# Kernel optimization log

Hardware: AMD Instinct MI355X
Metric: run time of the kernel (lower is better)

## Reference

```python
import jax, jax.numpy as jnp
import numpy as np

BN_EPS = 1e-5

def bn(x, gamma, beta):
    # x: [N, C]; BatchNorm2d over (batch, spatial) == node axis here (training-mode batch stats)
    mu = x.mean(axis=0, keepdims=True)
    var = x.var(axis=0, keepdims=True)
    return (x - mu) * jax.lax.rsqrt(var + BN_EPS) * gamma + beta

def octree_conv(x, neigh, W):
    # x: [N, Cin]; neigh: [N, K] with values in [0, N], N == empty neighbor
    # W: [K, Cin, Cout]. Sparse octree conv = neighbor gather + contraction.
    xp = jnp.concatenate([x, jnp.zeros((1, x.shape[1]), x.dtype)], axis=0)  # zero row for empties
    g = xp[neigh]                                  # [N, K, Cin]
    return jnp.einsum('nkc,kcd->nd', g, W)         # [N, Cout]

def setup_inputs() -> dict:
    key = jax.random.key(0)
    ks = jax.random.split(key, 8)
    N, Cin, Cout, Cb, K = 60000, 256, 512, 128, 27
    s = 0.05
    return {
        'x': jax.random.normal(ks[0], (1, Cin, N, 1), jnp.float32),
        'neigh': jax.random.randint(ks[1], (N, K), 0, N + 1),
        'W1a': jax.random.normal(ks[2], (Cb, Cin), jnp.float32) * s,
        'g1a': jnp.ones((Cb,), jnp.float32), 'b1a': jnp.zeros((Cb,), jnp.float32),
        'W3': jax.random.normal(ks[3], (K, Cb, Cb), jnp.float32) * s,
        'g3': jnp.ones((Cb,), jnp.float32), 'b3': jnp.zeros((Cb,), jnp.float32),
        'W1b': jax.random.normal(ks[4], (Cout, Cb), jnp.float32) * s,
        'g1b': jnp.ones((Cout,), jnp.float32), 'b1b': jnp.zeros((Cout,), jnp.float32),
        'Wc': jax.random.normal(ks[5], (Cout, Cin), jnp.float32) * s,
        'gc': jnp.ones((Cout,), jnp.float32), 'bc': jnp.zeros((Cout,), jnp.float32),
    }

def reference(x, neigh, W1a, g1a, b1a, W3, g3, b3, W1b, g1b, b1b, Wc, gc, bc):
    h = jnp.squeeze(x, axis=(0, 3)).T                         # [N, Cin]
    c1 = jax.nn.relu(bn(h @ W1a.T, g1a, b1a))                 # 1x1 conv + BN + ReLU -> [N, Cb]
    c2 = jax.nn.relu(bn(octree_conv(c1, neigh, W3), g3, b3))  # sparse 3x3 octree conv + BN + ReLU
    c3 = bn(c2 @ W1b.T, g1b, b1b)                             # 1x1 conv + BN -> [N, Cout]
    sc = bn(h @ Wc.T, gc, bc)                                 # shortcut 1x1 conv + BN (Cin != Cout)
    out = jax.nn.relu(c3 + sc)
    return out.T[None, :, :, None]                            # [1, Cout, N, 1]
```

## Files before the change

kernel.cpp:

```cpp
#include <hip/hip_runtime.h>


typedef __bf16 bf16x8 __attribute__((ext_vector_type(8)));
typedef float f32x4 __attribute__((ext_vector_type(4)));
typedef unsigned short u16x8 __attribute__((ext_vector_type(8)));
typedef unsigned short u16x4 __attribute__((ext_vector_type(4)));

__device__ __forceinline__ unsigned short f2bfu(float f) {
  union { float f; unsigned u; } v; v.f = f;
  unsigned r = v.u + 0x7fffu + ((v.u >> 16) & 1u);
  return (unsigned short)(r >> 16);
}
__device__ __forceinline__ float bfu2f(unsigned short s) {
  union { unsigned u; float f; } v; v.u = ((unsigned)s) << 16;
  return v.f;
}

__device__ __forceinline__ void gload_lds16(const unsigned short* g, unsigned short* l) {
  __builtin_amdgcn_global_load_lds(
      (const __attribute__((address_space(1))) unsigned int*)(unsigned long long)g,
      (__attribute__((address_space(3))) unsigned int*)(unsigned int)(unsigned long long)l,
      16, 0, 0);
}

__global__ __launch_bounds__(256) void prep_weights(
    const float* __restrict__ W1a, const float* __restrict__ W3,
    const float* __restrict__ W1b, const float* __restrict__ Wc,
    unsigned short* __restrict__ w1a, unsigned short* __restrict__ w3t,
    unsigned short* __restrict__ w1b, unsigned short* __restrict__ wc) {
  int i = blockIdx.x * 256 + threadIdx.x;
  int stride = gridDim.x * 256;
  for (; i < 442368; i += stride) {
    if (i < 32768)  w1a[i] = f2bfu(W1a[i]);
    if (i < 65536)  w1b[i] = f2bfu(W1b[i]);
    if (i < 131072) wc[i]  = f2bfu(Wc[i]);
    int k = i >> 14, rr = i & 16383;
    int d = rr >> 7, c = rr & 127;
    w3t[i] = f2bfu(W3[(k << 14) + (c << 7) + d]);
  }
}

__global__ __launch_bounds__(256) void transpose_x(
    const float* __restrict__ x, unsigned short* __restrict__ h, int M) {
  __shared__ float tile[64][65];
  int n0 = blockIdx.x * 64, c0 = blockIdx.y * 64;
  int t = threadIdx.x;
  int nl = t & 63;
#pragma unroll
  for (int i = 0; i < 16; ++i) {
    int cl = i * 4 + (t >> 6);
    int n = n0 + nl;
    tile[cl][nl] = (n < M) ? x[(size_t)(c0 + cl) * M + n] : 0.f;
  }
  __syncthreads();
  int cl = t & 63;
#pragma unroll
  for (int i = 0; i < 16; ++i) {
    int nl2 = i * 4 + (t >> 6);
    int n = n0 + nl2;
    h[(size_t)n * 256 + c0 + cl] = f2bfu(tile[cl][nl2]);
  }
}

__global__ __launch_bounds__(256) void gemm128(
    const unsigned short* __restrict__ A, const unsigned short* __restrict__ W,
    unsigned short* __restrict__ C, float* __restrict__ partials,
    int M, int Kd, int Nc) {
  __shared__ unsigned short sA[2][128 * 64];
  __shared__ unsigned short sB[2][128 * 64];
  __shared__ float sStat[4][2][128];
  int t = threadIdx.x, wave = t >> 6, lane = t & 63;
  int n0 = blockIdx.x * 128, m0 = blockIdx.y * 128;
  int wr = wave >> 1, wcc = wave & 1;
  int l4 = lane >> 4, lc = lane & 15, lc7 = lc & 7;
  int lrow = lane >> 3, lch = lane & 7;
  f32x4 acc[4][4] = {};
  const int np = Kd >> 6;

  auto STAGE = [&](int p, int buf) {
    int k0 = p << 6;
#pragma unroll
    for (int i = 0; i < 4; ++i) {
      int row = wave * 32 + i * 8 + lrow;
      int sc = lch ^ (row & 7);
      gload_lds16(A + (size_t)(m0 + row) * Kd + k0 + sc * 8, &sA[buf][(wave * 32 + i * 8) * 64]);
    }
#pragma unroll
    for (int i = 0; i < 4; ++i) {
      int row = wave * 32 + i * 8 + lrow;
      int sc = lch ^ (row & 7);
      gload_lds16(W + (size_t)(n0 + row) * Kd + k0 + sc * 8, &sB[buf][(wave * 32 + i * 8) * 64]);
    }
  };
  auto COMPUTE = [&](int buf) {
#pragma unroll
    for (int kk = 0; kk < 2; ++kk) {
      bf16x8 af[4], bfr[4];
#pragma unroll
      for (int mi = 0; mi < 4; ++mi) {
        int row = wr * 64 + mi * 16 + lc;
        int chunk = (kk * 4 + l4) ^ lc7;
        af[mi] = __builtin_bit_cast(bf16x8, *(const u16x8*)(&sA[buf][row * 64 + chunk * 8]));
      }
#pragma unroll
      for (int ni = 0; ni < 4; ++ni) {
        int row = wcc * 64 + ni * 16 + lc;
        int chunk = (kk * 4 + l4) ^ lc7;
        bfr[ni] = __builtin_bit_cast(bf16x8, *(const u16x8*)(&sB[buf][row * 64 + chunk * 8]));
      }
      __builtin_amdgcn_s_setprio(1);
#pragma unroll
      for (int mi = 0; mi < 4; ++mi)
#pragma unroll
        for (int ni = 0; ni < 4; ++ni)
          acc[mi][ni] = __builtin_amdgcn_mfma_f32_16x16x32_bf16(af[mi], bfr[ni], acc[mi][ni], 0, 0, 0);
      __builtin_amdgcn_s_setprio(0);
    }
  };

  STAGE(0, 0);
  for (int p = 0; p < np; ++p) {
    int cur = p & 1;
    if (p < np - 1) {
      STAGE(p + 1, cur ^ 1);
      asm volatile("s_waitcnt vmcnt(8)" ::: "memory");
    } else {
      asm volatile("s_waitcnt vmcnt(0)" ::: "memory");
    }
    __builtin_amdgcn_sched_barrier(0);
    __builtin_amdgcn_s_barrier();
    __builtin_amdgcn_sched_barrier(0);
    COMPUTE(cur);
    __builtin_amdgcn_sched_barrier(0);
    __builtin_amdgcn_s_barrier();
  }

#pragma unroll
  for (int ni = 0; ni < 4; ++ni) {
    float s = 0.f, q = 0.f;
    int col = wcc * 64 + ni * 16 + lc;
#pragma unroll
    for (int mi = 0; mi < 4; ++mi)
#pragma unroll
      for (int j = 0; j < 4; ++j) {
        int n = m0 + wr * 64 + mi * 16 + l4 * 4 + j;
        unsigned short u = f2bfu(acc[mi][ni][j]);
        if (n < M) C[(size_t)n * Nc + n0 + col] = u;
        float v = bfu2f(u);
        s += v; q += v * v;
      }
    s += __shfl_xor(s, 16); s += __shfl_xor(s, 32);
    q += __shfl_xor(q, 16); q += __shfl_xor(q, 32);
    if (lane < 16) {
      sStat[wave][0][col] = s;
      sStat[wave][1][col] = q;
    }
  }
  __syncthreads();
  if (t < 128) {
    int wcs = t >> 6;
    float s = sStat[wcs][0][t] + sStat[wcs + 2][0][t];
    float q = sStat[wcs][1][t] + sStat[wcs + 2][1][t];
    partials[(size_t)blockIdx.y * (2 * Nc) + n0 + t] = s;
    partials[(size_t)blockIdx.y * (2 * Nc) + Nc + n0 + t] = q;
  }
}

__global__ __launch_bounds__(512, 4) void octree_gemm(
    const unsigned short* __restrict__ c1, const int* __restrict__ neigh,
    const unsigned short* __restrict__ w3t, unsigned short* __restrict__ c2p,
    float* __restrict__ partials, int M) {
  __shared__ unsigned short sA[2][128 * 64];
  __shared__ unsigned short sB[2][128 * 64];
  __shared__ union {
    unsigned short nidx[128 * 27];
    float stat[8][2][128];
  } u;
  int t = threadIdx.x, wave = t >> 6, lane = t & 63;
  int m0 = blockIdx.x * 128;
  for (int i = t; i < 128 * 27; i += 512) {
    int row = i / 27;
    u.nidx[i] = (unsigned short)((m0 + row < M) ? neigh[(size_t)m0 * 27 + i] : M);
  }
  __syncthreads();

  int wr = wave >> 1, wcc = wave & 1;
  int l4 = lane >> 4, lc = lane & 15, lc7 = lc & 7;
  int lrow = lane >> 3, lch = lane & 7;
  f32x4 acc[2][4] = {};

  auto STAGE = [&](int p, int buf) {
    int k = p >> 1, c0 = (p & 1) << 6;
#pragma unroll
    for (int i = 0; i < 2; ++i) {
      int row = wave * 16 + i * 8 + lrow;
      int nr = u.nidx[row * 27 + k];
      int sc = lch ^ (row & 7);
      gload_lds16(c1 + ((size_t)nr << 7) + c0 + sc * 8, &sA[buf][(wave * 16 + i * 8) * 64]);
    }
    const unsigned short* wk = w3t + ((size_t)k << 14);
#pragma unroll
    for (int i = 0; i < 2; ++i) {
      int row = wave * 16 + i * 8 + lrow;
      int sc = lch ^ (row & 7);
      gload_lds16(wk + ((size_t)row << 7) + c0 + sc * 8, &sB[buf][(wave * 16 + i * 8) * 64]);
    }
  };
  auto COMPUTE = [&](int buf) {
#pragma unroll
    for (int kk = 0; kk < 2; ++kk) {
      bf16x8 af[2], bfr[4];
#pragma unroll
      for (int mi = 0; mi < 2; ++mi) {
        int row = wr * 32 + mi * 16 + lc;
        int chunk = (kk * 4 + l4) ^ lc7;
        af[mi] = __builtin_bit_cast(bf16x8, *(const u16x8*)(&sA[buf][row * 64 + chunk * 8]));
      }
#pragma unroll
      for (int ni = 0; ni < 4; ++ni) {
        int row = wcc * 64 + ni * 16 + lc;
        int chunk = (kk * 4 + l4) ^ lc7;
        bfr[ni] = __builtin_bit_cast(bf16x8, *(const u16x8*)(&sB[buf][row * 64 + chunk * 8]));
      }
      __builtin_amdgcn_s_setprio(1);
#pragma unroll
      for (int mi = 0; mi < 2; ++mi)
#pragma unroll
        for (int ni = 0; ni < 4; ++ni)
          acc[mi][ni] = __builtin_amdgcn_mfma_f32_16x16x32_bf16(af[mi], bfr[ni], acc[mi][ni], 0, 0, 0);
      __builtin_amdgcn_s_setprio(0);
    }
  };

  STAGE(0, 0);
  for (int p = 0; p < 54; ++p) {
    int cur = p & 1;
    if (p < 53) {
      STAGE(p + 1, cur ^ 1);
      asm volatile("s_waitcnt vmcnt(4)" ::: "memory");
    } else {
      asm volatile("s_waitcnt vmcnt(0)" ::: "memory");
    }
    __builtin_amdgcn_sched_barrier(0);
    __builtin_amdgcn_s_barrier();
    __builtin_amdgcn_sched_barrier(0);
    COMPUTE(cur);
    __builtin_amdgcn_sched_barrier(0);
    __builtin_amdgcn_s_barrier();
  }

#pragma unroll
  for (int ni = 0; ni < 4; ++ni) {
    float s = 0.f, q = 0.f;
    int col = wcc * 64 + ni * 16 + lc;
#pragma unroll
    for (int mi = 0; mi < 2; ++mi)
#pragma unroll
      for (int j = 0; j < 4; ++j) {
        int n = m0 + wr * 32 + mi * 16 + l4 * 4 + j;
        unsigned short uo = f2bfu(acc[mi][ni][j]);
        if (n < M) c2p[(size_t)n * 128 + col] = uo;
        float v = bfu2f(uo);
        s += v; q += v * v;
      }
    s += __shfl_xor(s, 16); s += __shfl_xor(s, 32);
    q += __shfl_xor(q, 16); q += __shfl_xor(q, 32);
    if (lane < 16) {
      u.stat[wave][0][col] = s;
      u.stat[wave][1][col] = q;
    }
  }
  __syncthreads();
  if (t < 128) {
    int wcs = t >> 6;
    float s = 0.f, q = 0.f;
#pragma unroll
    for (int g = 0; g < 4; ++g) {
      s += u.stat[g * 2 + wcs][0][t];
      q += u.stat[g * 2 + wcs][1][t];
    }
    partials[(size_t)blockIdx.x * 256 + t] = s;
    partials[(size_t)blockIdx.x * 256 + 128 + t] = q;
  }
}

__global__ __launch_bounds__(256) void bn_finalize(
    const float* __restrict__ partials, int nb, int C, int M,
    const float* __restrict__ g, const float* __restrict__ bt,
    float* __restrict__ ss) {
  int c = blockIdx.x;
  int t = threadIdx.x;
  float s = 0.f, s2 = 0.f;
  for (int b = t; b < nb; b += 256) {
    s += partials[(size_t)b * 2 * C + c];
    s2 += partials[(size_t)b * 2 * C + C + c];
  }
#pragma unroll
  for (int off = 32; off >= 1; off >>= 1) {
    s += __shfl_xor(s, off);
    s2 += __shfl_xor(s2, off);
  }
  __shared__ float sh[4][2];
  int wave = t >> 6, lane = t & 63;
  if (lane == 0) { sh[wave][0] = s; sh[wave][1] = s2; }
  __syncthreads();
  if (t == 0) {
    s = sh[0][0] + sh[1][0] + sh[2][0] + sh[3][0];
    s2 = sh[0][1] + sh[1][1] + sh[2][1] + sh[3][1];
    float mean = s / (float)M;
    float var = s2 / (float)M - mean * mean;
    float sc = g[c] * rsqrtf(var + 1e-5f);
    ss[c] = sc;
    ss[C + c] = bt[c] - mean * sc;
  }
}

__global__ __launch_bounds__(256) void bnrelu(
    const unsigned short* __restrict__ P, const float* __restrict__ ss,
    unsigned short* __restrict__ Aout, int total, int total2, int Cmask) {
  int i = (blockIdx.x * 256 + threadIdx.x) * 8;
  if (i >= total2) return;
  u16x8 o = {0, 0, 0, 0, 0, 0, 0, 0};
  if (i < total) {
    u16x8 v = *(const u16x8*)(P + i);
    int c0 = i & Cmask;
    int C = Cmask + 1;
#pragma unroll
    for (int j = 0; j < 8; ++j) {
      float f = bfu2f(v[j]) * ss[c0 + j] + ss[C + c0 + j];
      o[j] = f2bfu(fmaxf(f, 0.f));
    }
  }
  *(u16x8*)(Aout + i) = o;
}

__global__ __launch_bounds__(256) void final_out(
    const unsigned short* __restrict__ c3p, const unsigned short* __restrict__ scp,
    const float* __restrict__ ss3, const float* __restrict__ sssc,
    float* __restrict__ out, int M) {
  __shared__ float tile[64][129];
  int n0 = blockIdx.x * 64, c0 = blockIdx.y * 128;
  int t = threadIdx.x;
  int rowg = t >> 5, cg = (t & 31) * 4;
#pragma unroll
  for (int ps = 0; ps < 8; ++ps) {
    int nl = ps * 8 + rowg;
    int n = n0 + nl;
    float v0 = 0.f, v1 = 0.f, v2 = 0.f, v3 = 0.f;
    if (n < M) {
      u16x4 a = *(const u16x4*)(c3p + (size_t)n * 512 + c0 + cg);
      u16x4 b = *(const u16x4*)(scp + (size_t)n * 512 + c0 + cg);
      int c = c0 + cg;
      v0 = fmaxf(bfu2f(a[0]) * ss3[c + 0] + ss3[512 + c + 0] + bfu2f(b[0]) * sssc[c + 0] + sssc[512 + c + 0], 0.f);
      v1 = fmaxf(bfu2f(a[1]) * ss3[c + 1] + ss3[512 + c + 1] + bfu2f(b[1]) * sssc[c + 1] + sssc[512 + c + 1], 0.f);
      v2 = fmaxf(bfu2f(a[2]) * ss3[c + 2] + ss3[512 + c + 2] + bfu2f(b[2]) * sssc[c + 2] + sssc[512 + c + 2], 0.f);
      v3 = fmaxf(bfu2f(a[3]) * ss3[c + 3] + ss3[512 + c + 3] + bfu2f(b[3]) * sssc[c + 3] + sssc[512 + c + 3], 0.f);
    }
    tile[nl][cg + 0] = v0;
    tile[nl][cg + 1] = v1;
    tile[nl][cg + 2] = v2;
    tile[nl][cg + 3] = v3;
  }
  __syncthreads();
  int nl = t & 63, cq = t >> 6;
  int n = n0 + nl;
  if (n < M) {
#pragma unroll
    for (int i = 0; i < 32; ++i) {
      int cl = i * 4 + cq;
      out[(size_t)(c0 + cl) * M + n] = tile[nl][cl];
    }
  }
}

extern "C" void kernel_launch(void* const* d_in, const int* in_sizes, int n_in,
                              void* d_out, int out_size, void* d_ws, size_t ws_size,
                              hipStream_t stream) {
  const float* x   = (const float*)d_in[0];
  const int* neigh = (const int*)d_in[1];
  const float* W1a = (const float*)d_in[2];
  const float* g1a = (const float*)d_in[3];
  const float* b1a = (const float*)d_in[4];
  const float* W3  = (const float*)d_in[5];
  const float* g3  = (const float*)d_in[6];
  const float* b3  = (const float*)d_in[7];
  const float* W1b = (const float*)d_in[8];
  const float* g1b = (const float*)d_in[9];
  const float* b1b = (const float*)d_in[10];
  const float* Wc  = (const float*)d_in[11];
  const float* gc  = (const float*)d_in[12];
  const float* bc  = (const float*)d_in[13];
  float* out = (float*)d_out;

  const int M = in_sizes[1] / 27;
  const int MT = (M + 63) / 64;
  const int MTO = (M + 127) / 128;

  char* ws = (char*)d_ws;
  unsigned short* h   = (unsigned short*)(ws + 0);
  unsigned short* wA  = (unsigned short*)(ws + 30736384);
  unsigned short* wP  = (unsigned short*)(ws + 46104576);
  unsigned short* c3p = (unsigned short*)(ws + 61464576);
  unsigned short* scp = (unsigned short*)(ws + 122904576);
  unsigned short* w1a = (unsigned short*)(ws + 184344576);
  unsigned short* w3t = (unsigned short*)(ws + 184410112);
  unsigned short* w1b = (unsigned short*)(ws + 185294848);
  unsigned short* wc  = (unsigned short*)(ws + 185425920);
  float* ss1  = (float*)(ws + 185688064);
  float* ss2  = (float*)(ws + 185692160);
  float* ss3  = (float*)(ws + 185696256);
  float* sssc = (float*)(ws + 185700352);

  float* part12 = (float*)c3p;
  float* part3  = (float*)scp;
  float* partsc = (float*)wP;

  prep_weights<<<1728, 256, 0, stream>>>(W1a, W3, W1b, Wc, w1a, w3t, w1b, wc);
  transpose_x<<<dim3(MT, 4), 256, 0, stream>>>(x, h, M);

  const int total = M * 128, total2 = (MT * 64) * 128;
  const int bnGrid = (total2 / 8 + 255) / 256;

  gemm128<<<dim3(1, MTO), 256, 0, stream>>>(h, w1a, wP, part12, M, 256, 128);
  bn_finalize<<<128, 256, 0, stream>>>(part12, MTO, 128, M, g1a, b1a, ss1);
  bnrelu<<<bnGrid, 256, 0, stream>>>(wP, ss1, wA, total, total2, 127);

  octree_gemm<<<MTO, 512, 0, stream>>>(wA, neigh, w3t, wP, part12, M);
  bn_finalize<<<128, 256, 0, stream>>>(part12, MTO, 128, M, g3, b3, ss2);
  bnrelu<<<bnGrid, 256, 0, stream>>>(wP, ss2, wA, total, total2, 127);

  gemm128<<<dim3(4, MTO), 256, 0, stream>>>(wA, w1b, c3p, part3, M, 128, 512);
  bn_finalize<<<512, 256, 0, stream>>>(part3, MTO, 512, M, g1b, b1b, ss3);

  gemm128<<<dim3(4, MTO), 256, 0, stream>>>(h, wc, scp, partsc, M, 256, 512);
  bn_finalize<<<512, 256, 0, stream>>>(partsc, MTO, 512, M, gc, bc, sssc);

  final_out<<<dim3(MT, 4), 256, 0, stream>>>(c3p, scp, ss3, sssc, out, M);
}
```

Baseline: 250.2 us.

## Use 512-thread GEMM blocks and XCD-aware block swizzle for GEMM and octree kernels

The dense GEMM kernel moves from 4 waves to 8 waves per 128x128 tile, with each wave owning a 32x64 sub-tile, half the previous accumulator footprint. Staging loads are split across more waves and the vmcnt wait is adjusted to match. A 1D grid with an XCD-aware remap is added to both the GEMM and the octree kernel so that consecutive tiles land on the same XCD, aiming to improve L2 locality for shared weight and activation reads. The costs are more waves contending on the same LDS tile and extra index arithmetic.

```diff
diff --git a/kernel.cpp b/kernel.cpp
--- a/kernel.cpp
+++ b/kernel.cpp
@@ -21,6 +21,13 @@
       (const __attribute__((address_space(1))) unsigned int*)(unsigned long long)g,
       (__attribute__((address_space(3))) unsigned int*)(unsigned int)(unsigned long long)l,
       16, 0, 0);
+}
+
+__device__ __forceinline__ int xcd_swz(int bid, int nwg) {
+  int q = nwg >> 3, r = nwg & 7;
+  int xcd = bid & 7, idx = bid >> 3;
+  int base = xcd < r ? xcd * (q + 1) : r * (q + 1) + (xcd - r) * q;
+  return base + idx;
 }
 
 __global__ __launch_bounds__(256) void prep_weights(
@@ -62,43 +69,46 @@
   }
 }
 
-__global__ __launch_bounds__(256) void gemm128(
+__global__ __launch_bounds__(512, 4) void gemm128(
     const unsigned short* __restrict__ A, const unsigned short* __restrict__ W,
     unsigned short* __restrict__ C, float* __restrict__ partials,
-    int M, int Kd, int Nc) {
+    int M, int Kd, int Nc, int ncol) {
   __shared__ unsigned short sA[2][128 * 64];
   __shared__ unsigned short sB[2][128 * 64];
-  __shared__ float sStat[4][2][128];
+  __shared__ float sStat[8][2][128];
   int t = threadIdx.x, wave = t >> 6, lane = t & 63;
-  int n0 = blockIdx.x * 128, m0 = blockIdx.y * 128;
+  int flat = xcd_swz(blockIdx.x, gridDim.x);
+  int n0 = (flat % ncol) * 128;
+  int rowt = flat / ncol;
+  int m0 = rowt * 128;
   int wr = wave >> 1, wcc = wave & 1;
   int l4 = lane >> 4, lc = lane & 15, lc7 = lc & 7;
   int lrow = lane >> 3, lch = lane & 7;
-  f32x4 acc[4][4] = {};
+  f32x4 acc[2][4] = {};
   const int np = Kd >> 6;
 
   auto STAGE = [&](int p, int buf) {
     int k0 = p << 6;
 #pragma unroll
-    for (int i = 0; i < 4; ++i) {
-      int row = wave * 32 + i * 8 + lrow;
+    for (int i = 0; i < 2; ++i) {
+      int row = wave * 16 + i * 8 + lrow;
       int sc = lch ^ (row & 7);
-      gload_lds16(A + (size_t)(m0 + row) * Kd + k0 + sc * 8, &sA[buf][(wave * 32 + i * 8) * 64]);
-    }
-#pragma unroll
-    for (int i = 0; i < 4; ++i) {
-      int row = wave * 32 + i * 8 + lrow;
+      gload_lds16(A + (size_t)(m0 + row) * Kd + k0 + sc * 8, &sA[buf][(wave * 16 + i * 8) * 64]);
+    }
+#pragma unroll
+    for (int i = 0; i < 2; ++i) {
+      int row = wave * 16 + i * 8 + lrow;
       int sc = lch ^ (row & 7);
-      gload_lds16(W + (size_t)(n0 + row) * Kd + k0 + sc * 8, &sB[buf][(wave * 32 + i * 8) * 64]);
+      gload_lds16(W + (size_t)(n0 + row) * Kd + k0 + sc * 8, &sB[buf][(wave * 16 + i * 8) * 64]);
     }
   };
   auto COMPUTE = [&](int buf) {
 #pragma unroll
     for (int kk = 0; kk < 2; ++kk) {
-      bf16x8 af[4], bfr[4];
-#pragma unroll
-      for (int mi = 0; mi < 4; ++mi) {
-        int row = wr * 64 + mi * 16 + lc;
+      bf16x8 af[2], bfr[4];
+#pragma unroll
+      for (int mi = 0; mi < 2; ++mi) {
+        int row = wr * 32 + mi * 16 + lc;
         int chunk = (kk * 4 + l4) ^ lc7;
         af[mi] = __builtin_bit_cast(bf16x8, *(const u16x8*)(&sA[buf][row * 64 + chunk * 8]));
       }
@@ -110,7 +120,7 @@
       }
       __builtin_amdgcn_s_setprio(1);
 #pragma unroll
-      for (int mi = 0; mi < 4; ++mi)
+      for (int mi = 0; mi < 2; ++mi)
 #pragma unroll
         for (int ni = 0; ni < 4; ++ni)
           acc[mi][ni] = __builtin_amdgcn_mfma_f32_16x16x32_bf16(af[mi], bfr[ni], acc[mi][ni], 0, 0, 0);
@@ -123,7 +133,7 @@
     int cur = p & 1;
     if (p < np - 1) {
       STAGE(p + 1, cur ^ 1);
-      asm volatile("s_waitcnt vmcnt(8)" ::: "memory");
+      asm volatile("s_waitcnt vmcnt(4)" ::: "memory");
     } else {
       asm volatile("s_waitcnt vmcnt(0)" ::: "memory");
     }
@@ -140,10 +150,10 @@
     float s = 0.f, q = 0.f;
     int col = wcc * 64 + ni * 16 + lc;
 #pragma unroll
-    for (int mi = 0; mi < 4; ++mi)
+    for (int mi = 0; mi < 2; ++mi)
 #pragma unroll
       for (int j = 0; j < 4; ++j) {
-        int n = m0 + wr * 64 + mi * 16 + l4 * 4 + j;
+        int n = m0 + wr * 32 + mi * 16 + l4 * 4 + j;
         unsigned short u = f2bfu(acc[mi][ni][j]);
         if (n < M) C[(size_t)n * Nc + n0 + col] = u;
         float v = bfu2f(u);
@@ -159,10 +169,14 @@
   __syncthreads();
   if (t < 128) {
     int wcs = t >> 6;
-    float s = sStat[wcs][0][t] + sStat[wcs + 2][0][t];
-    float q = sStat[wcs][1][t] + sStat[wcs + 2][1][t];
-    partials[(size_t)blockIdx.y * (2 * Nc) + n0 + t] = s;
-    partials[(size_t)blockIdx.y * (2 * Nc) + Nc + n0 + t] = q;
+    float s = 0.f, q = 0.f;
+#pragma unroll
+    for (int g = 0; g < 4; ++g) {
+      s += sStat[g * 2 + wcs][0][t];
+      q += sStat[g * 2 + wcs][1][t];
+    }
+    partials[(size_t)rowt * (2 * Nc) + n0 + t] = s;
+    partials[(size_t)rowt * (2 * Nc) + Nc + n0 + t] = q;
   }
 }
 
@@ -177,7 +191,8 @@
     float stat[8][2][128];
   } u;
   int t = threadIdx.x, wave = t >> 6, lane = t & 63;
-  int m0 = blockIdx.x * 128;
+  int rowt = xcd_swz(blockIdx.x, gridDim.x);
+  int m0 = rowt * 128;
   for (int i = t; i < 128 * 27; i += 512) {
     int row = i / 27;
     u.nidx[i] = (unsigned short)((m0 + row < M) ? neigh[(size_t)m0 * 27 + i] : M);
@@ -279,8 +294,8 @@
       s += u.stat[g * 2 + wcs][0][t];
       q += u.stat[g * 2 + wcs][1][t];
     }
-    partials[(size_t)blockIdx.x * 256 + t] = s;
-    partials[(size_t)blockIdx.x * 256 + 128 + t] = q;
+    partials[(size_t)rowt * 256 + t] = s;
+    partials[(size_t)rowt * 256 + 128 + t] = q;
   }
 }
 
@@ -421,7 +436,7 @@
   const int total = M * 128, total2 = (MT * 64) * 128;
   const int bnGrid = (total2 / 8 + 255) / 256;
 
-  gemm128<<<dim3(1, MTO), 256, 0, stream>>>(h, w1a, wP, part12, M, 256, 128);
+  gemm128<<<MTO, 512, 0, stream>>>(h, w1a, wP, part12, M, 256, 128, 1);
   bn_finalize<<<128, 256, 0, stream>>>(part12, MTO, 128, M, g1a, b1a, ss1);
   bnrelu<<<bnGrid, 256, 0, stream>>>(wP, ss1, wA, total, total2, 127);
 
@@ -429,10 +444,10 @@
   bn_finalize<<<128, 256, 0, stream>>>(part12, MTO, 128, M, g3, b3, ss2);
   bnrelu<<<bnGrid, 256, 0, stream>>>(wP, ss2, wA, total, total2, 127);
 
-  gemm128<<<dim3(4, MTO), 256, 0, stream>>>(wA, w1b, c3p, part3, M, 128, 512);
+  gemm128<<<4 * MTO, 512, 0, stream>>>(wA, w1b, c3p, part3, M, 128, 512, 4);
   bn_finalize<<<512, 256, 0, stream>>>(part3, MTO, 512, M, g1b, b1b, ss3);
 
-  gemm128<<<dim3(4, MTO), 256, 0, stream>>>(h, wc, scp, partsc, M, 256, 512);
+  gemm128<<<4 * MTO, 512, 0, stream>>>(h, wc, scp, partsc, M, 256, 512, 4);
   bn_finalize<<<512, 256, 0, stream>>>(partsc, MTO, 512, M, gc, bc, sssc);
 
   final_out<<<dim3(MT, 4), 256, 0, stream>>>(c3p, scp, ss3, sssc, out, M);
```

New measurement: 237.1 us. -5.2%, faster.
